# Optimization experiments

Hardware: AMD Instinct MI355X
Metric: run time of the kernel (lower is better)

Reference implementation:

```python
import jax, jax.numpy as jnp
import numpy as np

ORDER, IN_DIM, OUT_DIM, SEQ_LEN = 4096, 8, 1, 4096


def setup_inputs() -> dict:
    key = jax.random.key(0)
    ks = jax.random.split(key, 7)
    # reset_parameter uses uniform(-0.7, 0.7); A/C/L rescaled ~1/sqrt(order) for
    # numerical stability of the 4096-step linear recurrence (same math, stable values).
    sA = 0.9 * (3.0 / ORDER) ** 0.5
    sC = 0.7 / ORDER ** 0.5
    weight_a = jax.random.uniform(ks[0], (ORDER, ORDER), minval=-sA, maxval=sA, dtype=jnp.float32)
    weight_b = jax.random.uniform(ks[1], (ORDER, IN_DIM), minval=-0.7, maxval=0.7, dtype=jnp.float32)
    weight_c = jax.random.uniform(ks[2], (OUT_DIM, ORDER), minval=-sC, maxval=sC, dtype=jnp.float32)
    weight_d = jax.random.uniform(ks[3], (OUT_DIM, IN_DIM), minval=-0.7, maxval=0.7, dtype=jnp.float32)
    weight_l = jax.random.uniform(ks[4], (ORDER, 1), minval=-sC, maxval=sC, dtype=jnp.float32)
    u = jax.random.normal(ks[5], (IN_DIM, SEQ_LEN), dtype=jnp.float32)
    y_obs = jax.random.normal(ks[6], (1, SEQ_LEN), dtype=jnp.float32)
    return {"u": u, "y_obs": y_obs, "weight_a": weight_a, "weight_b": weight_b,
            "weight_c": weight_c, "weight_d": weight_d, "weight_l": weight_l}


def reference(u, y_obs, weight_a, weight_b, weight_c, weight_d, weight_l):
    # Observer (Luenberger) state-space recursion, inp_dim > 1 branch:
    #   y_t  = C h_t + D u_t
    #   h_{t+1} = A h_t + B u_t + L * (y_obs_t - y_t)
    # output = tanh(concat(y_t)) * 3, shape [out_dim, seq_len]
    order = weight_a.shape[0]
    h0 = jnp.ones((order, 1), dtype=u.dtype)  # nn.init.constant_(hidden, 1)

    def step(h, inp):
        u_t, yobs_t = inp  # u_t: [in_dim, 1], yobs_t: scalar
        y_t = weight_c @ h + weight_d @ u_t          # [out_dim, 1]
        h_next = weight_a @ h + weight_b @ u_t + weight_l * (yobs_t - y_t)
        return h_next, y_t

    u_seq = u.T[:, :, None]          # [seq_len, in_dim, 1]
    _, ys = jax.lax.scan(step, h0, (u_seq, y_obs[0]))
    y_hat = ys[:, :, 0].T            # [out_dim, seq_len]
    return jnp.tanh(y_hat) * 3
```

## Files before the change

kernel.cpp:

```cpp
#include <hip/hip_runtime.h>
#include <math.h>


constexpr int NDIM  = 4096;
constexpr int NC    = 10;
constexpr int SLAB  = 16 * 4096;
constexpr int JT    = 56;
constexpr int VAPPS = 28;
constexpr int RAPPS = 27;
constexpr int KC    = NDIM / 32;
constexpr int TILES = NDIM / 16;

typedef float    f32x4  __attribute__((ext_vector_type(4)));
typedef _Float16 h16x8  __attribute__((ext_vector_type(8)));
typedef _Float16 f16;

__global__ __launch_bounds__(256) void k_build_a(
        const float* __restrict__ A, const float* __restrict__ C,
        const float* __restrict__ L,
        h16x8* __restrict__ AhSw, f16* __restrict__ At) {
    __shared__ float lds[64][65];
    const int R0 = (blockIdx.x & 63) * 64;
    const int C0 = (blockIdx.x >> 6) * 64;
    const int tid = threadIdx.x;
    #pragma unroll
    for (int it = 0; it < 16; ++it) {
        const int r = it * 4 + (tid >> 6);
        const int c = tid & 63;
        lds[r][c] = A[(size_t)(R0 + r) * NDIM + C0 + c]
                  - L[R0 + r] * C[C0 + c];
    }
    __syncthreads();
    #pragma unroll
    for (int it = 0; it < 16; ++it) {
        const int c = it * 4 + (tid >> 6);
        const int r = tid & 63;
        At[(size_t)(C0 + c) * NDIM + R0 + r] = (f16)lds[r][c];
    }
    #pragma unroll
    for (int half = 0; half < 2; ++half) {
        const int o = half * 256 + tid;
        const int r = o >> 3;
        const int g = o & 7;
        union { h16x8 v; f16 h[8]; } pk;
        #pragma unroll
        for (int j = 0; j < 8; ++j) pk.h[j] = (f16)lds[r][g * 8 + j];
        const int tile = (R0 >> 4) + (r >> 4);
        const int kc   = (C0 >> 5) + (g >> 2);
        const int lane = (r & 15) | ((g & 3) << 4);
        AhSw[((size_t)tile * KC + kc) * 64 + lane] = pk.v;
    }
}

__global__ __launch_bounds__(256) void k_build_w0(
        const float* __restrict__ Bm, const float* __restrict__ Dm,
        const float* __restrict__ L, const float* __restrict__ C,
        float* __restrict__ Wf, f16* __restrict__ Wh, float* __restrict__ gf) {
    int k = blockIdx.x * blockDim.x + threadIdx.x;
    float Lk = L[k];
    float col[16];
    #pragma unroll
    for (int c = 0; c < 8; ++c) col[c] = Bm[k * 8 + c] - Lk * Dm[c];
    col[8] = Lk; col[9] = 1.0f;
    #pragma unroll
    for (int c = 10; c < 16; ++c) col[c] = 0.0f;
    #pragma unroll
    for (int c = 0; c < 16; ++c) {
        Wf[c * NDIM + k] = col[c];
        Wh[c * NDIM + k] = (f16)col[c];
    }
    gf[k] = C[k];
}

__global__ __launch_bounds__(256) void k_stepVR(
        const h16x8* __restrict__ AhSw, const f16* __restrict__ At,
        const f16* __restrict__ WhIn,
        float* __restrict__ WfOut, f16* __restrict__ WhOut,
        const float* __restrict__ gIn, float* __restrict__ gOut,
        const int doR) {
    __shared__ f32x4 red[4][64];
    const int tid = threadIdx.x;

    if (blockIdx.x < 256) {
        const int lane = tid & 63, wave = tid >> 6;
        const int mr   = lane & 15, q = lane >> 4;
        const int tile = blockIdx.x;
        const int row0 = tile * 16;
        const int k0   = wave * 1024;
        const bool liveB = (mr < NC);
        const h16x8* a8 = AhSw + ((size_t)tile * KC + wave * 32) * 64 + lane;
        const h16x8* b8 = (const h16x8*)WhIn + (((size_t)mr * NDIM + k0) >> 3) + q;

        f32x4 acc0 = {0,0,0,0}, acc1 = {0,0,0,0};
        for (int it = 0; it < 4; ++it) {
            h16x8 ra[8], rb[8];
            #pragma unroll
            for (int s = 0; s < 8; ++s) rb[s] = (h16x8){0,0,0,0,0,0,0,0};
            #pragma unroll
            for (int s = 0; s < 8; ++s) {
                const int c = it * 8 + s;
                ra[s] = a8[(size_t)c * 64];
            }
            if (liveB) {
                #pragma unroll
                for (int s = 0; s < 8; ++s) {
                    const int c = it * 8 + s;
                    rb[s] = b8[c * 4];
                }
            }
            #pragma unroll
            for (int s = 0; s < 8; ++s) {
                if (s & 1) acc1 = __builtin_amdgcn_mfma_f32_16x16x32_f16(ra[s], rb[s], acc1, 0, 0, 0);
                else       acc0 = __builtin_amdgcn_mfma_f32_16x16x32_f16(ra[s], rb[s], acc0, 0, 0, 0);
            }
        }
        red[wave][lane] = acc0 + acc1;
        __syncthreads();
        if (tid < 64) {
            f32x4 v = red[0][tid] + red[1][tid] + red[2][tid] + red[3][tid];
            const int col = tid & 15;
            if (col < NC) {
                const int rb0 = row0 + ((tid >> 4) << 2);
                #pragma unroll
                for (int i = 0; i < 4; ++i) {
                    WfOut[col * NDIM + rb0 + i] = v[i];
                    WhOut[col * NDIM + rb0 + i] = (f16)v[i];
                }
            }
        }
    } else {
        if (!doR) return;
        const int tile = blockIdx.x - 256;
        const int rl   = tid >> 4;
        const int l16  = tid & 15;
        const size_t rowg = (size_t)tile * 16 + rl;
        const h16x8* arow = (const h16x8*)(At + rowg * NDIM) + l16;
        const f32x4* g4   = (const f32x4*)gIn + l16 * 2;
        float acc = 0.0f;
        #pragma unroll 4
        for (int j = 0; j < 32; ++j) {
            union { h16x8 v; f16 h[8]; } ua;
            ua.v = arow[j * 16];
            f32x4 g0 = g4[j * 32];
            f32x4 g1 = g4[j * 32 + 1];
            #pragma unroll
            for (int e = 0; e < 4; ++e)
                acc += (float)ua.h[e] * g0[e] + (float)ua.h[e + 4] * g1[e];
        }
        #pragma unroll
        for (int off = 8; off > 0; off >>= 1) acc += __shfl_down(acc, off, 16);
        if (l16 == 0) gOut[rowg] = acc;
    }
}

__global__ __launch_bounds__(256) void k_fbatch(
        const float* __restrict__ Wall, const float* __restrict__ C,
        const float* __restrict__ gf, float* __restrict__ F) {
    const int m = blockIdx.x;
    const float* W;
    const float* vec;
    if (m <= VAPPS) { W = Wall + (size_t)m * SLAB;     vec = C; }
    else            { W = Wall + (size_t)VAPPS * SLAB; vec = gf + (size_t)(m - VAPPS) * NDIM; }
    const int tid = threadIdx.x, lane = tid & 63, wave = tid >> 6;
    float acc[NC] = {};
    for (int k = tid; k < NDIM; k += 256) {
        float ck = vec[k];
        #pragma unroll
        for (int c = 0; c < NC; ++c) acc[c] += ck * W[c * NDIM + k];
    }
    __shared__ float red[4][NC];
    #pragma unroll
    for (int c = 0; c < NC; ++c) {
        float s = acc[c];
        #pragma unroll
        for (int off = 32; off > 0; off >>= 1) s += __shfl_down(s, off);
        if (lane == 0) red[wave][c] = s;
    }
    __syncthreads();
    if (tid < NC) F[m * NC + tid] = red[0][tid] + red[1][tid] + red[2][tid] + red[3][tid];
}

__global__ __launch_bounds__(256) void k_conv(
        const float* __restrict__ F, const float* __restrict__ u,
        const float* __restrict__ yobs, const float* __restrict__ Dm,
        float* __restrict__ out) {
    __shared__ float Fl[JT * NC];
    __shared__ float zw[(JT + 256) * 9];
    const int tid = threadIdx.x;
    const int t0  = blockIdx.x * 256;
    for (int idx = tid; idx < JT * NC; idx += 256) Fl[idx] = F[idx];
    for (int idx = tid; idx < (JT + 256) * 9; idx += 256) {
        int k = idx / 9, c = idx - k * 9;
        int s = t0 - JT + k;
        float v = 0.0f;
        if (s >= 0 && s < NDIM) v = (c < 8) ? u[c * NDIM + s] : yobs[s];
        zw[idx] = v;
    }
    __syncthreads();
    const int t = t0 + tid;
    float y = (t < JT) ? Fl[t * NC + 9] : 0.0f;
    #pragma unroll
    for (int c = 0; c < 8; ++c) y += Dm[c] * u[c * NDIM + t];
    for (int j = 0; j < JT; ++j) {
        const float* fj = Fl + j * NC;
        const float* zz = zw + (tid + JT - 1 - j) * 9;
        float p = 0.0f;
        #pragma unroll
        for (int c = 0; c < 9; ++c) p += fj[c] * zz[c];
        y += p;
    }
    out[t] = 3.0f * tanhf(y);
}

extern "C" void kernel_launch(void* const* d_in, const int* in_sizes, int n_in,
                              void* d_out, int out_size, void* d_ws, size_t ws_size,
                              hipStream_t stream) {
    const float* u    = (const float*)d_in[0];
    const float* yobs = (const float*)d_in[1];
    const float* A    = (const float*)d_in[2];
    const float* Bm   = (const float*)d_in[3];
    const float* C    = (const float*)d_in[4];
    const float* Dm   = (const float*)d_in[5];
    const float* L    = (const float*)d_in[6];
    float* out = (float*)d_out;

    char* ws = (char*)d_ws;
    h16x8* AhSw = (h16x8*)ws;
    f16*   At   = (f16*)(ws + 33554432ull);
    float* Wf   = (float*)(ws + 67108864ull);
    f16*   Wh   = (f16*)(ws + 74711040ull);
    float* gf   = (float*)(ws + 78512128ull);
    float* F    = (float*)(ws + 78970880ull);

    k_build_a<<<dim3(64 * 64), dim3(256), 0, stream>>>(A, C, L, AhSw, At);
    k_build_w0<<<dim3(16), dim3(256), 0, stream>>>(Bm, Dm, L, C, Wf, Wh, gf);

    for (int r = 0; r < VAPPS; ++r) {
        const size_t in   = (size_t)r * SLAB;
        const size_t out_ = (size_t)(r + 1) * SLAB;
        const int doR = (r < RAPPS) ? 1 : 0;
        k_stepVR<<<dim3(512), dim3(256), 0, stream>>>(
            AhSw, At, Wh + in, Wf + out_, Wh + out_,
            gf + (size_t)r * NDIM, gf + (size_t)(r + 1) * NDIM, doR);
    }

    k_fbatch<<<dim3(JT), dim3(256), 0, stream>>>(Wf, C, gf, F);
    k_conv<<<dim3(16), dim3(256), 0, stream>>>(F, u, yobs, Dm, out);
}
```

Measured before the change: 482.6 us.

## Drop transposed A copy; compute row-vector products from swizzled A with split-K partials

The build kernel no longer writes a transposed fp16 copy of A-LC. It becomes a simple vectorized pass that produces only the MFMA-swizzled layout, removing half the setup writes and the LDS transpose. The g^T·A chain now reads the swizzled tiles directly. Each block produces per-tile partial sums into a double-buffered Rpart buffer, and the next launch reduces them through LDS. The cost is an extra 4 MB partial buffer written and read on every step.

```diff
diff --git a/kernel.cpp b/kernel.cpp
--- a/kernel.cpp
+++ b/kernel.cpp
@@ -7,7 +7,6 @@
 constexpr int SLAB  = 16 * 4096;
 constexpr int JT    = 56;
 constexpr int VAPPS = 28;
-constexpr int RAPPS = 27;
 constexpr int KC    = NDIM / 32;
 constexpr int TILES = NDIM / 16;
 
@@ -17,45 +16,32 @@
 
 __global__ __launch_bounds__(256) void k_build_a(
         const float* __restrict__ A, const float* __restrict__ C,
-        const float* __restrict__ L,
-        h16x8* __restrict__ AhSw, f16* __restrict__ At) {
-    __shared__ float lds[64][65];
-    const int R0 = (blockIdx.x & 63) * 64;
-    const int C0 = (blockIdx.x >> 6) * 64;
-    const int tid = threadIdx.x;
-    #pragma unroll
-    for (int it = 0; it < 16; ++it) {
-        const int r = it * 4 + (tid >> 6);
-        const int c = tid & 63;
-        lds[r][c] = A[(size_t)(R0 + r) * NDIM + C0 + c]
-                  - L[R0 + r] * C[C0 + c];
-    }
-    __syncthreads();
-    #pragma unroll
-    for (int it = 0; it < 16; ++it) {
-        const int c = it * 4 + (tid >> 6);
-        const int r = tid & 63;
-        At[(size_t)(C0 + c) * NDIM + R0 + r] = (f16)lds[r][c];
-    }
-    #pragma unroll
-    for (int half = 0; half < 2; ++half) {
-        const int o = half * 256 + tid;
-        const int r = o >> 3;
-        const int g = o & 7;
-        union { h16x8 v; f16 h[8]; } pk;
-        #pragma unroll
-        for (int j = 0; j < 8; ++j) pk.h[j] = (f16)lds[r][g * 8 + j];
-        const int tile = (R0 >> 4) + (r >> 4);
-        const int kc   = (C0 >> 5) + (g >> 2);
-        const int lane = (r & 15) | ((g & 3) << 4);
-        AhSw[((size_t)tile * KC + kc) * 64 + lane] = pk.v;
-    }
+        const float* __restrict__ L, h16x8* __restrict__ AhSw) {
+    const size_t idx = (size_t)blockIdx.x * blockDim.x + threadIdx.x;
+    const int lane = (int)(idx & 63);
+    const int kc   = (int)((idx >> 6) & (KC - 1));
+    const int tile = (int)(idx >> 13);
+    const int row  = tile * 16 + (lane & 15);
+    const int col  = kc * 32 + (lane >> 4) * 8;
+    const float4 a0 = *(const float4*)(A + (size_t)row * NDIM + col);
+    const float4 a1 = *(const float4*)(A + (size_t)row * NDIM + col + 4);
+    const float Li = L[row];
+    union { h16x8 v; f16 h[8]; } pk;
+    pk.h[0] = (f16)(a0.x - Li * C[col + 0]);
+    pk.h[1] = (f16)(a0.y - Li * C[col + 1]);
+    pk.h[2] = (f16)(a0.z - Li * C[col + 2]);
+    pk.h[3] = (f16)(a0.w - Li * C[col + 3]);
+    pk.h[4] = (f16)(a1.x - Li * C[col + 4]);
+    pk.h[5] = (f16)(a1.y - Li * C[col + 5]);
+    pk.h[6] = (f16)(a1.z - Li * C[col + 6]);
+    pk.h[7] = (f16)(a1.w - Li * C[col + 7]);
+    AhSw[idx] = pk.v;
 }
 
 __global__ __launch_bounds__(256) void k_build_w0(
         const float* __restrict__ Bm, const float* __restrict__ Dm,
-        const float* __restrict__ L, const float* __restrict__ C,
-        float* __restrict__ Wf, f16* __restrict__ Wh, float* __restrict__ gf) {
+        const float* __restrict__ L,
+        float* __restrict__ Wf, f16* __restrict__ Wh) {
     int k = blockIdx.x * blockDim.x + threadIdx.x;
     float Lk = L[k];
     float col[16];
@@ -69,19 +55,18 @@
         Wf[c * NDIM + k] = col[c];
         Wh[c * NDIM + k] = (f16)col[c];
     }
-    gf[k] = C[k];
 }
 
 __global__ __launch_bounds__(256) void k_stepVR(
-        const h16x8* __restrict__ AhSw, const f16* __restrict__ At,
-        const f16* __restrict__ WhIn,
+        const h16x8* __restrict__ AhSw, const f16* __restrict__ WhIn,
         float* __restrict__ WfOut, f16* __restrict__ WhOut,
-        const float* __restrict__ gIn, float* __restrict__ gOut,
-        const int doR) {
-    __shared__ f32x4 red[4][64];
+        const float* __restrict__ Cvec,
+        const float* __restrict__ RpartIn, float* __restrict__ RpartOut,
+        float* __restrict__ gfSlot, const int r) {
     const int tid = threadIdx.x;
 
     if (blockIdx.x < 256) {
+        __shared__ f32x4 red[4][64];
         const int lane = tid & 63, wave = tid >> 6;
         const int mr   = lane & 15, q = lane >> 4;
         const int tile = blockIdx.x;
@@ -129,27 +114,63 @@
             }
         }
     } else {
-        if (!doR) return;
-        const int tile = blockIdx.x - 256;
-        const int rl   = tid >> 4;
-        const int l16  = tid & 15;
-        const size_t rowg = (size_t)tile * 16 + rl;
-        const h16x8* arow = (const h16x8*)(At + rowg * NDIM) + l16;
-        const f32x4* g4   = (const f32x4*)gIn + l16 * 2;
-        float acc = 0.0f;
-        #pragma unroll 4
-        for (int j = 0; j < 32; ++j) {
-            union { h16x8 v; f16 h[8]; } ua;
-            ua.v = arow[j * 16];
-            f32x4 g0 = g4[j * 32];
-            f32x4 g1 = g4[j * 32 + 1];
-            #pragma unroll
-            for (int e = 0; e < 4; ++e)
-                acc += (float)ua.h[e] * g0[e] + (float)ua.h[e + 4] * g1[e];
-        }
-        #pragma unroll
-        for (int off = 8; off > 0; off >>= 1) acc += __shfl_down(acc, off, 16);
-        if (l16 == 0) gOut[rowg] = acc;
+        __shared__ float rp[256][17];
+        __shared__ float g2[16][17];
+        __shared__ float gs[16];
+        const int t = blockIdx.x - 256;
+
+        if (r == 0) {
+            if (tid < 16) gs[tid] = Cvec[t * 16 + tid];
+        } else {
+            const float* src = RpartIn + (size_t)tid * NDIM + t * 16;
+            #pragma unroll
+            for (int j = 0; j < 16; j += 4) {
+                float4 v = *(const float4*)(src + j);
+                rp[tid][j] = v.x; rp[tid][j+1] = v.y;
+                rp[tid][j+2] = v.z; rp[tid][j+3] = v.w;
+            }
+            __syncthreads();
+            {
+                const int c = tid & 15, g = tid >> 4;
+                float p = 0.0f;
+                #pragma unroll
+                for (int j = 0; j < 16; ++j) p += rp[g * 16 + j][c];
+                g2[g][c] = p;
+            }
+            __syncthreads();
+            if (tid < 16) {
+                float s = 0.0f;
+                #pragma unroll
+                for (int g = 0; g < 16; ++g) s += g2[g][tid];
+                gs[tid] = s;
+            }
+        }
+        __syncthreads();
+        if (tid < 16) gfSlot[t * 16 + tid] = gs[tid];
+
+        if (r < VAPPS - 1) {
+            float gloc[16];
+            #pragma unroll
+            for (int j = 0; j < 16; ++j) gloc[j] = gs[j];
+            const h16x8* base = AhSw + (size_t)t * (KC * 64);
+            #pragma unroll
+            for (int cc = 0; cc < 2; ++cc) {
+                const int ch = tid * 2 + cc;
+                const h16x8* fr = base + (size_t)ch * 16;
+                float acc[8] = {};
+                #pragma unroll
+                for (int mrr = 0; mrr < 16; ++mrr) {
+                    union { h16x8 v; f16 h[8]; } ua;
+                    ua.v = fr[mrr];
+                    const float gm = gloc[mrr];
+                    #pragma unroll
+                    for (int j = 0; j < 8; ++j) acc[j] += gm * (float)ua.h[j];
+                }
+                float4* op = (float4*)(RpartOut + (size_t)t * NDIM + 8 * ch);
+                op[0] = make_float4(acc[0], acc[1], acc[2], acc[3]);
+                op[1] = make_float4(acc[4], acc[5], acc[6], acc[7]);
+            }
+        }
     }
 }
 
@@ -225,23 +246,26 @@
     float* out = (float*)d_out;
 
     char* ws = (char*)d_ws;
-    h16x8* AhSw = (h16x8*)ws;
-    f16*   At   = (f16*)(ws + 33554432ull);
-    float* Wf   = (float*)(ws + 67108864ull);
-    f16*   Wh   = (f16*)(ws + 74711040ull);
-    float* gf   = (float*)(ws + 78512128ull);
-    float* F    = (float*)(ws + 78970880ull);
-
-    k_build_a<<<dim3(64 * 64), dim3(256), 0, stream>>>(A, C, L, AhSw, At);
-    k_build_w0<<<dim3(16), dim3(256), 0, stream>>>(Bm, Dm, L, C, Wf, Wh, gf);
+    h16x8* AhSw  = (h16x8*)ws;
+    float* Wf    = (float*)(ws + 33554432ull);
+    f16*   Wh    = (f16*)(ws + 41156608ull);
+    float* gf    = (float*)(ws + 44957696ull);
+    float* Rpart = (float*)(ws + 45416448ull);
+    float* F     = (float*)(ws + 53805056ull);
+
+    constexpr size_t RPN = (size_t)256 * NDIM;
+
+    k_build_a<<<dim3(TILES * KC * 64 / 256), dim3(256), 0, stream>>>(A, C, L, AhSw);
+    k_build_w0<<<dim3(16), dim3(256), 0, stream>>>(Bm, Dm, L, Wf, Wh);
 
     for (int r = 0; r < VAPPS; ++r) {
         const size_t in   = (size_t)r * SLAB;
         const size_t out_ = (size_t)(r + 1) * SLAB;
-        const int doR = (r < RAPPS) ? 1 : 0;
+        const float* rin  = Rpart + ((r + 1) & 1) * RPN;
+        float*       rout = Rpart + (r & 1) * RPN;
         k_stepVR<<<dim3(512), dim3(256), 0, stream>>>(
-            AhSw, At, Wh + in, Wf + out_, Wh + out_,
-            gf + (size_t)r * NDIM, gf + (size_t)(r + 1) * NDIM, doR);
+            AhSw, Wh + in, Wf + out_, Wh + out_,
+            C, rin, rout, gf + (size_t)r * NDIM, r);
     }
 
     k_fbatch<<<dim3(JT), dim3(256), 0, stream>>>(Wf, C, gf, F);
```

Result: faster. 470.8 us (-2.4%).
